# Kernel tuning notes

Measured on AMD Instinct MI355X. Metric: run time of the kernel, lower is better.

## Reference

```python
import jax, jax.numpy as jnp
import numpy as np

N_NODES = 100000
N_EDGES = 3200000


def setup_inputs() -> dict:
    key = jax.random.key(0)
    k1, k2, k3, k4 = jax.random.split(key, 4)
    x = jax.random.normal(k1, (N_NODES, 58), dtype=jnp.float32)
    edge_index = jax.random.randint(k2, (2, N_EDGES), 0, N_NODES, dtype=jnp.int64)
    # Xavier-uniform(gain=1.414) linear weights, zero biases (per reset_parameters)
    def xavier(k, fan_out, fan_in, gain=1.414):
        a = gain * np.sqrt(6.0 / (fan_in + fan_out))
        return jax.random.uniform(k, (fan_out, fan_in), minval=-a, maxval=a, dtype=jnp.float32)
    W1 = xavier(k3, 16, 58)
    b1 = jnp.zeros((16,), dtype=jnp.float32)
    W2 = xavier(k4, 1, 16)
    b2 = jnp.zeros((1,), dtype=jnp.float32)
    return {"x": x, "edge_index": edge_index, "W1": W1, "b1": b1, "W2": W2, "b2": b2}


def _mean_conv(h, edge_index, num_nodes):
    # SimpleConv(aggr='mean'): out[i] = mean over edges (src -> dst=i) of h[src]
    src, dst = edge_index[0], edge_index[1]
    summed = jax.ops.segment_sum(h[src], dst, num_segments=num_nodes)  # [N, d]
    cnt = jax.ops.segment_sum(jnp.ones((edge_index.shape[1],), h.dtype), dst,
                              num_segments=num_nodes)                  # [N]
    return summed / jnp.maximum(cnt, 1.0)[:, None]


def reference(x, edge_index, W1, b1, W2, b2):
    # Inference-mode PMLP (training=False): dropout is identity, norm=None.
    n = x.shape[0]
    # layer 0: linear -> mean graph conv -> bias -> relu
    h = x @ W1.T                      # [N, 16]
    h = _mean_conv(h, edge_index, n)  # [N, 16]
    h = jax.nn.relu(h + b1)
    # layer 1 (last): linear -> bias
    out = h @ W2.T + b2               # [N, 1]
    return out
```

## Files before the change

### kernel.cpp

```cpp
#include <hip/hip_runtime.h>
#include <hip/hip_fp16.h>

#define N_NODES 100000
#define N_EDGES 3200000
#define NBKT 782
#define EB 512
#define EPB (N_EDGES / EB)
#define SCAN_BLOCK 512
#define NSCAN (NBKT * EB)
#define NB_SCAN ((NSCAN + SCAN_BLOCK - 1) / SCAN_BLOCK)
#define SORT_CAP 5120
#define LIN_BLOCKS ((N_NODES + 511) / 512)


__global__ void lin_hist_kernel(const float* __restrict__ x,
                                const float* __restrict__ W1,
                                __half2* __restrict__ h2,
                                const int* __restrict__ ei32,
                                const long long* __restrict__ ei64,
                                int* __restrict__ bcount) {
    __shared__ float w[16 * 58];
    __shared__ int hist[NBKT];
    __shared__ int dflag;
    int tid = threadIdx.x;

    if (blockIdx.x < LIN_BLOCKS) {
        for (int idx = tid; idx < 16 * 58; idx += 512) w[idx] = W1[idx];
        __syncthreads();

        int i = blockIdx.x * 512 + tid;
        if (i >= N_NODES) return;

        float xv[58];
        const float* xr = x + (long)i * 58;
#pragma unroll
        for (int k = 0; k < 58; ++k) xv[k] = xr[k];

        __half2 o[8];
#pragma unroll
        for (int q = 0; q < 8; ++q) {
            float a[2];
#pragma unroll
            for (int r = 0; r < 2; ++r) {
                int c = q * 2 + r;
                float acc = 0.0f;
#pragma unroll
                for (int k = 0; k < 58; ++k) acc += xv[k] * w[c * 58 + k];
                a[r] = acc;
            }
            o[q] = __floats2half2_rn(a[0], a[1]);
        }
        float4* dst = (float4*)(h2 + (long)i * 8);
        float4* src = (float4*)o;
        dst[0] = src[0];
        dst[1] = src[1];
    } else {
        int blk = blockIdx.x - LIN_BLOCKS;
        if (tid == 0) dflag = 0;
        for (int i = tid; i < NBKT; i += 512) hist[i] = 0;
        __syncthreads();
        if (((const unsigned int*)ei32)[2 * tid + 1] != 0u) atomicOr(&dflag, 1);
        __syncthreads();
        bool i64 = (dflag == 0);

        long base = (long)blk * EPB;
        for (int k = tid; k < EPB; k += 512) {
            long e = base + k;
            int dst = i64 ? (int)ei64[N_EDGES + e] : ei32[N_EDGES + e];
            atomicAdd(&hist[dst >> 7], 1);
        }
        __syncthreads();
        for (int b = tid; b < NBKT; b += 512)
            bcount[(long)b * EB + blk] = hist[b];
    }
}

__global__ void scan1_kernel(int* __restrict__ data,
                             int* __restrict__ bsums, int n) {
    __shared__ int tmp[SCAN_BLOCK];
    int i = blockIdx.x * SCAN_BLOCK + threadIdx.x;
    int v = (i < n) ? data[i] : 0;
    tmp[threadIdx.x] = v;
    __syncthreads();
#pragma unroll
    for (int d = 1; d < SCAN_BLOCK; d <<= 1) {
        int t = (threadIdx.x >= d) ? tmp[threadIdx.x - d] : 0;
        __syncthreads();
        tmp[threadIdx.x] += t;
        __syncthreads();
    }
    if (i < n) data[i] = tmp[threadIdx.x] - v;
    if (threadIdx.x == SCAN_BLOCK - 1) bsums[blockIdx.x] = tmp[threadIdx.x];
}

__global__ void scan2_kernel(int* __restrict__ bsums, int nb) {
    __shared__ int tmp[1024];
    int i = threadIdx.x;
    int v = (i < nb) ? bsums[i] : 0;
    tmp[i] = v;
    __syncthreads();
#pragma unroll
    for (int d = 1; d < 1024; d <<= 1) {
        int t = (i >= d) ? tmp[i - d] : 0;
        __syncthreads();
        tmp[i] += t;
        __syncthreads();
    }
    if (i < nb) bsums[i] = tmp[i] - v;
}

__global__ void __launch_bounds__(1024, 8)
scatter_sort_kernel(const int* __restrict__ ei32,
                    const long long* __restrict__ ei64,
                    const int* __restrict__ bcount,
                    const int* __restrict__ bsums,
                    unsigned int* __restrict__ packed) {
    __shared__ unsigned int vals[EPB];
    __shared__ unsigned int dstin[EPB];
    __shared__ unsigned short bjs[EPB];
    __shared__ int hist[NBKT];
    __shared__ int curs[NBKT];
    __shared__ int gbase[NBKT];
    __shared__ int tmp[1024];
    __shared__ int dflag;

    int tid = threadIdx.x;
    if (tid == 0) dflag = 0;
    for (int i = tid; i < NBKT; i += 1024) hist[i] = 0;
    __syncthreads();
    if (tid < 512 && ((const unsigned int*)ei32)[2 * tid + 1] != 0u)
        atomicOr(&dflag, 1);
    __syncthreads();
    bool i64 = (dflag == 0);
    long base = (long)blockIdx.x * EPB;

    for (int k = tid; k < EPB; k += 1024) {
        long e = base + k;
        int dst = i64 ? (int)ei64[N_EDGES + e] : ei32[N_EDGES + e];
        dstin[k] = (unsigned int)dst;
        atomicAdd(&hist[dst >> 7], 1);
    }
    __syncthreads();

    int v = (tid < NBKT) ? hist[tid] : 0;
    tmp[tid] = v;
    __syncthreads();
#pragma unroll
    for (int d = 1; d < 1024; d <<= 1) {
        int t = (tid >= d) ? tmp[tid - d] : 0;
        __syncthreads();
        tmp[tid] += t;
        __syncthreads();
    }
    if (tid < NBKT) {
        int s = tmp[tid] - v;
        long gi = (long)tid * EB + blockIdx.x;
        curs[tid] = s;
        gbase[tid] = bcount[gi] + bsums[gi >> 9] - s;
    }
    __syncthreads();

    for (int k = tid; k < EPB; k += 1024) {
        long e = base + k;
        int src = i64 ? (int)ei64[e] : ei32[e];
        unsigned int dst = dstin[k];
        int b = (int)(dst >> 7);
        int p = atomicAdd(&curs[b], 1);
        vals[p] = ((dst & 127u) << 17) | (unsigned int)src;
        bjs[p] = (unsigned short)b;
    }
    __threadfence_block();
    __syncthreads();

    for (int j = tid; j < EPB; j += 1024)
        packed[gbase[bjs[j]] + j] = vals[j];
}

__global__ void __launch_bounds__(1024, 2)
sort_gather_kernel(const unsigned int* __restrict__ packed,
                   const int* __restrict__ bcount,
                   const int* __restrict__ bsums,
                   const __half2* __restrict__ h2,
                   const float* __restrict__ b1,
                   const float* __restrict__ W2,
                   const float* __restrict__ b2,
                   float* __restrict__ out) {
    __shared__ unsigned int raw[SORT_CAP];
    __shared__ unsigned int sortedv[SORT_CAP];
    __shared__ int hist[128];
    __shared__ int starts[128];
    __shared__ int curs[128];
    __shared__ int tmp[1024];

    int b = blockIdx.x;
    int tid = threadIdx.x;
    long gi = (long)b * EB;
    int start = bcount[gi] + bsums[gi >> 9];
    int end;
    if (b + 1 < NBKT) {
        long gj = (long)(b + 1) * EB;
        end = bcount[gj] + bsums[gj >> 9];
    } else {
        end = N_EDGES;
    }
    int m = end - start;
    bool fast = (m <= SORT_CAP);

    if (tid < 128) hist[tid] = 0;
    __syncthreads();

    if (fast) {
        for (int k = tid; k < m; k += 1024) raw[k] = packed[start + k];
        __syncthreads();
        for (int k = tid; k < m; k += 1024)
            atomicAdd(&hist[(int)(raw[k] >> 17)], 1);
    } else {
        for (int k = tid; k < m; k += 1024)
            atomicAdd(&hist[(int)(packed[start + k] >> 17)], 1);
    }
    __syncthreads();

    int v = (tid < 128) ? hist[tid] : 0;
    tmp[tid] = v;
    __syncthreads();
#pragma unroll
    for (int d = 1; d < 128; d <<= 1) {
        int t = (tid >= d) ? tmp[tid - d] : 0;
        __syncthreads();
        tmp[tid] += t;
        __syncthreads();
    }
    if (tid < 128) {
        int s = tmp[tid] - v;
        starts[tid] = s;
        curs[tid] = s;
    }
    __syncthreads();

    if (fast) {
        for (int k = tid; k < m; k += 1024) {
            unsigned int w = raw[k];
            int l = (int)(w >> 17);
            int p = atomicAdd(&curs[l], 1);
            sortedv[p] = w & 0x1FFFFu;
        }
        __threadfence_block();
    }
    __syncthreads();

    int l = tid >> 3;
    int c = tid & 7;
    int g = b * 128 + l;
    if (g >= N_NODES) return;

    int deg = hist[l];
    float2 acc0 = {0.0f, 0.0f}, acc1 = {0.0f, 0.0f};

    if (fast) {
        int p = starts[l], pend = p + deg;
        for (; p + 3 < pend; p += 4) {
            int sA = (int)sortedv[p];
            int sB = (int)sortedv[p + 1];
            int sC = (int)sortedv[p + 2];
            int sD = (int)sortedv[p + 3];
            float2 fA = __half22float2(h2[(long)sA * 8 + c]);
            float2 fB = __half22float2(h2[(long)sB * 8 + c]);
            float2 fC = __half22float2(h2[(long)sC * 8 + c]);
            float2 fD = __half22float2(h2[(long)sD * 8 + c]);
            acc0.x += fA.x + fC.x; acc0.y += fA.y + fC.y;
            acc1.x += fB.x + fD.x; acc1.y += fB.y + fD.y;
        }
        for (; p < pend; ++p) {
            float2 f = __half22float2(h2[(long)sortedv[p] * 8 + c]);
            acc0.x += f.x; acc0.y += f.y;
        }
    } else {
        for (int p = start; p < end; ++p) {
            unsigned int w = packed[p];
            if ((int)(w >> 17) == l) {
                float2 f = __half22float2(h2[(long)(w & 0x1FFFFu) * 8 + c]);
                acc0.x += f.x; acc0.y += f.y;
            }
        }
    }

    float inv = 1.0f / fmaxf((float)deg, 1.0f);
    float sx = acc0.x + acc1.x, sy = acc0.y + acc1.y;
    float vv = fmaxf(sx * inv + b1[2 * c], 0.0f)     * W2[2 * c]
             + fmaxf(sy * inv + b1[2 * c + 1], 0.0f) * W2[2 * c + 1];
    vv += __shfl_xor(vv, 1);
    vv += __shfl_xor(vv, 2);
    vv += __shfl_xor(vv, 4);
    if (c == 0) out[g] = vv + b2[0];
}

__global__ void detect_i64_kernel(const unsigned int* __restrict__ ei,
                                  unsigned int* __restrict__ flag) {
    unsigned int v = 0;
    int lane = threadIdx.x;
    for (int j = lane; j < 512; j += 64) v |= ei[2 * j + 1];
    unsigned long long any_nonzero = __ballot(v != 0u);
    if (lane == 0) *flag = (any_nonzero == 0ULL) ? 1u : 0u;
}

__global__ void linear1_f32_kernel(const float* __restrict__ x,
                                   const float* __restrict__ W1,
                                   float* __restrict__ h, int n) {
    __shared__ float w[16 * 58];
    for (int idx = threadIdx.x; idx < 16 * 58; idx += blockDim.x)
        w[idx] = W1[idx];
    __syncthreads();
    int i = blockIdx.x * blockDim.x + threadIdx.x;
    if (i >= n) return;
    float xv[58];
    const float* xr = x + (long)i * 58;
#pragma unroll
    for (int k = 0; k < 58; ++k) xv[k] = xr[k];
#pragma unroll
    for (int cq = 0; cq < 4; ++cq) {
        float a[4];
#pragma unroll
        for (int r = 0; r < 4; ++r) {
            int ch = cq * 4 + r;
            float acc = 0.0f;
#pragma unroll
            for (int k = 0; k < 58; ++k) acc += xv[k] * w[ch * 58 + k];
            a[r] = acc;
        }
        ((float4*)(h + (long)i * 16))[cq] = make_float4(a[0], a[1], a[2], a[3]);
    }
}

__global__ void scatter_kernel(const int* __restrict__ ei32,
                               const long long* __restrict__ ei64,
                               const unsigned int* __restrict__ flag,
                               const float* __restrict__ h,
                               float* __restrict__ summed,
                               float* __restrict__ cnt) {
    long e = (long)blockIdx.x * blockDim.x + threadIdx.x;
    if (e >= N_EDGES) return;
    long src, dst;
    if (*flag) { src = (long)ei64[e]; dst = (long)ei64[N_EDGES + e]; }
    else       { src = (long)ei32[e]; dst = (long)ei32[N_EDGES + e]; }
    const float4* hs = (const float4*)(h + src * 16);
    float4 a = hs[0], b = hs[1], c = hs[2], d = hs[3];
    float* o = summed + dst * 16;
    atomicAdd(o + 0,  a.x); atomicAdd(o + 1,  a.y);
    atomicAdd(o + 2,  a.z); atomicAdd(o + 3,  a.w);
    atomicAdd(o + 4,  b.x); atomicAdd(o + 5,  b.y);
    atomicAdd(o + 6,  b.z); atomicAdd(o + 7,  b.w);
    atomicAdd(o + 8,  c.x); atomicAdd(o + 9,  c.y);
    atomicAdd(o + 10, c.z); atomicAdd(o + 11, c.w);
    atomicAdd(o + 12, d.x); atomicAdd(o + 13, d.y);
    atomicAdd(o + 14, d.z); atomicAdd(o + 15, d.w);
    atomicAdd(cnt + dst, 1.0f);
}

__global__ void finalize_kernel(const float* __restrict__ summed,
                                const float* __restrict__ cnt,
                                const float* __restrict__ b1,
                                const float* __restrict__ W2,
                                const float* __restrict__ b2,
                                float* __restrict__ out, int n) {
    int i = blockIdx.x * blockDim.x + threadIdx.x;
    if (i >= n) return;
    const float4* s = (const float4*)(summed + (long)i * 16);
    float4 s0 = s[0], s1 = s[1], s2 = s[2], s3 = s[3];
    float sv[16] = {s0.x, s0.y, s0.z, s0.w, s1.x, s1.y, s1.z, s1.w,
                    s2.x, s2.y, s2.z, s2.w, s3.x, s3.y, s3.z, s3.w};
    float inv = 1.0f / fmaxf(cnt[i], 1.0f);
    float acc = b2[0];
#pragma unroll
    for (int c = 0; c < 16; ++c)
        acc += W2[c] * fmaxf(sv[c] * inv + b1[c], 0.0f);
    out[i] = acc;
}

extern "C" void kernel_launch(void* const* d_in, const int* in_sizes, int n_in,
                              void* d_out, int out_size, void* d_ws, size_t ws_size,
                              hipStream_t stream) {
    const float* x  = (const float*)d_in[0];
    const void*  ei = d_in[1];
    const float* W1 = (const float*)d_in[2];
    const float* b1 = (const float*)d_in[3];
    const float* W2 = (const float*)d_in[4];
    const float* b2 = (const float*)d_in[5];
    float* out = (float*)d_out;

    float* ws = (float*)d_ws;

    const size_t need_bkt =
        (size_t)(800000 + 3200000 + NSCAN + 1024) * 4;

    if (ws_size >= need_bkt) {
        __half2*      h2     = (__half2*)ws;
        unsigned int* packed = (unsigned int*)(ws + 800000);
        int*          bcount = (int*)(ws + 800000 + 3200000);
        int*          bsums  = bcount + NSCAN;

        lin_hist_kernel<<<LIN_BLOCKS + EB, 512, 0, stream>>>(
            x, W1, h2, (const int*)ei, (const long long*)ei, bcount);

        scan1_kernel<<<NB_SCAN, SCAN_BLOCK, 0, stream>>>(bcount, bsums, NSCAN);
        scan2_kernel<<<1, 1024, 0, stream>>>(bsums, NB_SCAN);

        scatter_sort_kernel<<<EB, 1024, 0, stream>>>(
            (const int*)ei, (const long long*)ei, bcount, bsums, packed);

        sort_gather_kernel<<<NBKT, 1024, 0, stream>>>(
            packed, bcount, bsums, h2, b1, W2, b2, out);
    } else {
        float* h      = ws;
        float* summed = ws + N_NODES * 16;
        float* cnt    = ws + N_NODES * 32;
        unsigned int* flag = (unsigned int*)(ws + N_NODES * 33);

        hipMemsetAsync(summed, 0, (size_t)(N_NODES * 17) * sizeof(float), stream);
        detect_i64_kernel<<<1, 64, 0, stream>>>((const unsigned int*)ei, flag);
        linear1_f32_kernel<<<(N_NODES + 127) / 128, 128, 0, stream>>>(x, W1, h, N_NODES);
        scatter_kernel<<<(N_EDGES + 255) / 256, 256, 0, stream>>>(
            (const int*)ei, (const long long*)ei, flag, h, summed, cnt);
        finalize_kernel<<<(N_NODES + 255) / 256, 256, 0, stream>>>(
            summed, cnt, b1, W2, b2, out, N_NODES);
    }
}
```

Before: 77.61 us.

## Replace LDS scans with wavefront shuffle scans and fold scan2 into consumers

Adds a block-wide exclusive scan built on 64-lane shuffles plus a per-wavefront sums array, replacing the shared-memory Hillis-Steele scans that used two barriers per step. The separate single-block scan2 launch is removed. scatter_sort and sort_gather now each rescan the 782 per-bucket block sums themselves, which works because each scan1 block covers exactly one bucket row. This cuts one kernel launch and many barriers, at the cost of redundant small scans in every block of the two downstream kernels.

```diff
diff --git a/kernel.cpp b/kernel.cpp
--- a/kernel.cpp
+++ b/kernel.cpp
@@ -12,6 +12,33 @@
 #define SORT_CAP 5120
 #define LIN_BLOCKS ((N_NODES + 511) / 512)
 
+template <int NT>
+__device__ __forceinline__ int block_excl_scan(int v, int tid, int* wsum) {
+    __syncthreads();
+    int lane = tid & 63;
+    int w = tid >> 6;
+    int incl = v;
+#pragma unroll
+    for (int d = 1; d < 64; d <<= 1) {
+        int t = __shfl_up(incl, d, 64);
+        if (lane >= d) incl += t;
+    }
+    if (lane == 63) wsum[w] = incl;
+    __syncthreads();
+    if (w == 0) {
+        constexpr int NW = NT / 64;
+        int s = (lane < NW) ? wsum[lane] : 0;
+        int si = s;
+#pragma unroll
+        for (int d = 1; d < NW; d <<= 1) {
+            int t = __shfl_up(si, d, 64);
+            if (lane >= d) si += t;
+        }
+        if (lane < NW) wsum[lane] = si - s;
+    }
+    __syncthreads();
+    return incl - v + wsum[w];
+}
 
 __global__ void lin_hist_kernel(const float* __restrict__ x,
                                 const float* __restrict__ W1,
@@ -75,38 +102,14 @@
     }
 }
 
-__global__ void scan1_kernel(int* __restrict__ data,
-                             int* __restrict__ bsums, int n) {
-    __shared__ int tmp[SCAN_BLOCK];
+__global__ void __launch_bounds__(SCAN_BLOCK)
+scan1_kernel(int* __restrict__ data, int* __restrict__ bsums, int n) {
+    __shared__ int wsum[16];
     int i = blockIdx.x * SCAN_BLOCK + threadIdx.x;
     int v = (i < n) ? data[i] : 0;
-    tmp[threadIdx.x] = v;
-    __syncthreads();
-#pragma unroll
-    for (int d = 1; d < SCAN_BLOCK; d <<= 1) {
-        int t = (threadIdx.x >= d) ? tmp[threadIdx.x - d] : 0;
-        __syncthreads();
-        tmp[threadIdx.x] += t;
-        __syncthreads();
-    }
-    if (i < n) data[i] = tmp[threadIdx.x] - v;
-    if (threadIdx.x == SCAN_BLOCK - 1) bsums[blockIdx.x] = tmp[threadIdx.x];
-}
-
-__global__ void scan2_kernel(int* __restrict__ bsums, int nb) {
-    __shared__ int tmp[1024];
-    int i = threadIdx.x;
-    int v = (i < nb) ? bsums[i] : 0;
-    tmp[i] = v;
-    __syncthreads();
-#pragma unroll
-    for (int d = 1; d < 1024; d <<= 1) {
-        int t = (i >= d) ? tmp[i - d] : 0;
-        __syncthreads();
-        tmp[i] += t;
-        __syncthreads();
-    }
-    if (i < nb) bsums[i] = tmp[i] - v;
+    int excl = block_excl_scan<SCAN_BLOCK>(v, threadIdx.x, wsum);
+    if (i < n) data[i] = excl;
+    if (threadIdx.x == SCAN_BLOCK - 1) bsums[blockIdx.x] = excl + v;
 }
 
 __global__ void __launch_bounds__(1024, 8)
@@ -121,7 +124,7 @@
     __shared__ int hist[NBKT];
     __shared__ int curs[NBKT];
     __shared__ int gbase[NBKT];
-    __shared__ int tmp[1024];
+    __shared__ int wsum[16];
     __shared__ int dflag;
 
     int tid = threadIdx.x;
@@ -142,21 +145,14 @@
     }
     __syncthreads();
 
-    int v = (tid < NBKT) ? hist[tid] : 0;
-    tmp[tid] = v;
-    __syncthreads();
-#pragma unroll
-    for (int d = 1; d < 1024; d <<= 1) {
-        int t = (tid >= d) ? tmp[tid - d] : 0;
-        __syncthreads();
-        tmp[tid] += t;
-        __syncthreads();
-    }
+    int hv = (tid < NBKT) ? hist[tid] : 0;
+    int lexcl = block_excl_scan<1024>(hv, tid, wsum);
+    int bv = (tid < NBKT) ? bsums[tid] : 0;
+    int sb = block_excl_scan<1024>(bv, tid, wsum);
     if (tid < NBKT) {
-        int s = tmp[tid] - v;
         long gi = (long)tid * EB + blockIdx.x;
-        curs[tid] = s;
-        gbase[tid] = bcount[gi] + bsums[gi >> 9] - s;
+        curs[tid] = lexcl;
+        gbase[tid] = bcount[gi] + sb - lexcl;
     }
     __syncthreads();
 
@@ -178,7 +174,6 @@
 
 __global__ void __launch_bounds__(1024, 2)
 sort_gather_kernel(const unsigned int* __restrict__ packed,
-                   const int* __restrict__ bcount,
                    const int* __restrict__ bsums,
                    const __half2* __restrict__ h2,
                    const float* __restrict__ b1,
@@ -190,24 +185,23 @@
     __shared__ int hist[128];
     __shared__ int starts[128];
     __shared__ int curs[128];
-    __shared__ int tmp[1024];
+    __shared__ int wsum[16];
+    __shared__ int bounds[2];
 
     int b = blockIdx.x;
     int tid = threadIdx.x;
-    long gi = (long)b * EB;
-    int start = bcount[gi] + bsums[gi >> 9];
-    int end;
-    if (b + 1 < NBKT) {
-        long gj = (long)(b + 1) * EB;
-        end = bcount[gj] + bsums[gj >> 9];
-    } else {
-        end = N_EDGES;
-    }
+
+    if (tid < 128) hist[tid] = 0;
+
+    int bv = (tid < NBKT) ? bsums[tid] : 0;
+    int sb = block_excl_scan<1024>(bv, tid, wsum);
+    if (tid == b) { bounds[0] = sb; bounds[1] = sb + bv; }
+    __syncthreads();
+
+    int start = bounds[0];
+    int end = bounds[1];
     int m = end - start;
     bool fast = (m <= SORT_CAP);
-
-    if (tid < 128) hist[tid] = 0;
-    __syncthreads();
 
     if (fast) {
         for (int k = tid; k < m; k += 1024) raw[k] = packed[start + k];
@@ -220,20 +214,11 @@
     }
     __syncthreads();
 
-    int v = (tid < 128) ? hist[tid] : 0;
-    tmp[tid] = v;
-    __syncthreads();
-#pragma unroll
-    for (int d = 1; d < 128; d <<= 1) {
-        int t = (tid >= d) ? tmp[tid - d] : 0;
-        __syncthreads();
-        tmp[tid] += t;
-        __syncthreads();
-    }
+    int hv = (tid < 128) ? hist[tid] : 0;
+    int nexcl = block_excl_scan<1024>(hv, tid, wsum);
     if (tid < 128) {
-        int s = tmp[tid] - v;
-        starts[tid] = s;
-        curs[tid] = s;
+        starts[tid] = nexcl;
+        curs[tid] = nexcl;
     }
     __syncthreads();
 
@@ -402,13 +387,12 @@
             x, W1, h2, (const int*)ei, (const long long*)ei, bcount);
 
         scan1_kernel<<<NB_SCAN, SCAN_BLOCK, 0, stream>>>(bcount, bsums, NSCAN);
-        scan2_kernel<<<1, 1024, 0, stream>>>(bsums, NB_SCAN);
 
         scatter_sort_kernel<<<EB, 1024, 0, stream>>>(
             (const int*)ei, (const long long*)ei, bcount, bsums, packed);
 
         sort_gather_kernel<<<NBKT, 1024, 0, stream>>>(
-            packed, bcount, bsums, h2, b1, W2, b2, out);
+            packed, bsums, h2, b1, W2, b2, out);
     } else {
         float* h      = ws;
         float* summed = ws + N_NODES * 16;
```

Result: faster. 73.34 us (-5.5%).
